# Performance work log

Measured on AMD Instinct MI355X. Metric: run time of the kernel, lower is better.

Reference implementation:

```python
import jax, jax.numpy as jnp
import numpy as np

V, D, H, DK, DV = 60000, 300, 15, 20, 20
B, NH, NC, L = 128, 50, 5, 30
HD = H * DV  # 300, equals d_model
A = 200      # additive attention hidden dim


def _encode(x, Wq, Wk, Wv, Wp, bp, qv):
    # NRMS news/user encoder: MHSA over positions + additive attention pooling.
    # x: [B, L, D] -> [B, HD]
    b, l, _ = x.shape
    q = (x @ Wq).reshape(b, l, H, DK)
    k = (x @ Wk).reshape(b, l, H, DK)
    v = (x @ Wv).reshape(b, l, H, DV)
    scores = jnp.einsum('blhk,bmhk->bhlm', q, k) / jnp.sqrt(jnp.asarray(DK, x.dtype))
    attn = jax.nn.softmax(scores, axis=-1)
    ctx = jnp.einsum('bhlm,bmhv->blhv', attn, v).reshape(b, l, HD)
    a = jax.nn.softmax(jnp.tanh(ctx @ Wp + bp) @ qv, axis=-1)  # [b, l]
    return jnp.einsum('bl,blc->bc', a, ctx)

# vectorize over the per-position encoder axis (replaces the Python loop +
# incremental torch.cat): inputs [B, P, L, D], weights have leading dim P.
_encode_pos = jax.vmap(_encode, in_axes=(1, 0, 0, 0, 0, 0, 0), out_axes=1)


def setup_inputs() -> dict:
    key = jax.random.key(0)
    ks = jax.random.split(key, 24)

    def mk(k, shape, s=0.02):
        return s * jax.random.normal(k, shape, jnp.float32)

    inp = {
        'news_input': jax.random.randint(ks[0], (B, NH, L), 0, V),
        'candidates': jax.random.randint(ks[1], (B, NC, L), 0, V),
        'emb': mk(ks[2], (V, D), 0.1),
    }
    for name, n, base in [('his', NH, 3), ('cand', NC, 10), ('usr', 0, 17)]:
        sh = (n,) if n else ()
        kk = jax.random.split(ks[base], 6)
        inp[name + '_Wq'] = mk(kk[0], sh + (D, H * DK))
        inp[name + '_Wk'] = mk(kk[1], sh + (D, H * DK))
        inp[name + '_Wv'] = mk(kk[2], sh + (D, H * DV))
        inp[name + '_Wp'] = mk(kk[3], sh + (HD, A))
        inp[name + '_bp'] = mk(kk[4], sh + (A,))
        inp[name + '_qv'] = mk(kk[5], sh + (A,))
    return inp


def reference(news_input, candidates, emb,
              his_Wq, his_Wk, his_Wv, his_Wp, his_bp, his_qv,
              cand_Wq, cand_Wk, cand_Wv, cand_Wp, cand_bp, cand_qv,
              usr_Wq, usr_Wk, usr_Wv, usr_Wp, usr_bp, usr_qv):
    news_emb = emb[news_input]   # [B, 50, L, D]
    cand_emb = emb[candidates]   # [B, 5, L, D]
    news_enc = _encode_pos(news_emb, his_Wq, his_Wk, his_Wv, his_Wp, his_bp, his_qv)    # [B, 50, 300]
    cand_enc = _encode_pos(cand_emb, cand_Wq, cand_Wk, cand_Wv, cand_Wp, cand_bp, cand_qv)  # [B, 5, 300]
    user_rep = _encode(news_enc, usr_Wq, usr_Wk, usr_Wv, usr_Wp, usr_bp, usr_qv)        # [B, 300]
    scores = jnp.einsum('bd,bcd->bc', user_rep, cand_enc)  # bmm of [B,1,300] x [B,300,5]
    return jax.nn.softmax(scores, axis=-1)
```

## Files before the change

kernel.cpp:

```cpp
#include <hip/hip_runtime.h>
#include <math.h>

typedef __attribute__((ext_vector_type(8))) short short8;
typedef __attribute__((ext_vector_type(4))) short short4v;
typedef __attribute__((ext_vector_type(4))) float f32x4;

union U32S8 { unsigned u[4]; short8 s8; ushort e[8]; short4v h[2]; };

#define BATCH 128
#define NHIS  50
#define NCAND 5
#define KP    320
#define NQKV  1024
#define NWP   208
#define NQK   640
#define CTS   320
#define VOCAB 60000
#define SCALE 0.22360679774997896f

__device__ __forceinline__ ushort f2bf(float f) {
    union { float f; unsigned u; } v; v.f = f;
    return (ushort)((v.u + 0x7fffu + ((v.u >> 16) & 1u)) >> 16);
}
__device__ __forceinline__ unsigned pack2bf(float lo, float hi) {
    return (unsigned)f2bf(lo) | ((unsigned)f2bf(hi) << 16);
}
__device__ __forceinline__ float bf2f(ushort u) {
    union { float f; unsigned u; } v; v.u = ((unsigned)u) << 16;
    return v.f;
}

__device__ __forceinline__ void gl_lds16(const ushort* gsrc, ushort* ldst) {
    __builtin_amdgcn_global_load_lds(
        (const __attribute__((address_space(1))) unsigned int*)gsrc,
        (__attribute__((address_space(3))) unsigned int*)ldst,
        16, 0, 0);
}

__global__ void prep_emb(const float* __restrict__ emb, ushort* __restrict__ dst) {
    size_t gid = (size_t)blockIdx.x * 256 + threadIdx.x;
    size_t total8 = (size_t)VOCAB * (KP / 8);
    if (gid >= total8) return;
    size_t e0 = gid * 8;
    int row = (int)(e0 / KP);
    int c   = (int)(e0 - (size_t)row * KP);
    unsigned w[4] = {0, 0, 0, 0};
    if (c + 8 <= 300) {
        const float4* s = (const float4*)(emb + (size_t)row * 300 + c);
        float4 v0 = s[0], v1 = s[1];
        w[0] = pack2bf(v0.x, v0.y); w[1] = pack2bf(v0.z, v0.w);
        w[2] = pack2bf(v1.x, v1.y); w[3] = pack2bf(v1.z, v1.w);
    } else if (c < 300) {
        const float* s = emb + (size_t)row * 300;
        ushort tmp[8];
        #pragma unroll
        for (int i = 0; i < 8; ++i) tmp[i] = (c + i < 300) ? f2bf(s[c + i]) : (ushort)0;
        w[0] = tmp[0] | ((unsigned)tmp[1] << 16);
        w[1] = tmp[2] | ((unsigned)tmp[3] << 16);
        w[2] = tmp[4] | ((unsigned)tmp[5] << 16);
        w[3] = tmp[6] | ((unsigned)tmp[7] << 16);
    }
    *(unsigned*)(dst + e0)     = w[0];
    *(unsigned*)(dst + e0 + 2) = w[1];
    *(unsigned*)(dst + e0 + 4) = w[2];
    *(unsigned*)(dst + e0 + 6) = w[3];
}

__global__ void prep_qkv(const float* __restrict__ Wq, const float* __restrict__ Wk,
                         const float* __restrict__ Wv, ushort* __restrict__ dst, int P) {
    size_t i = (size_t)blockIdx.x * 256 + threadIdx.x;
    size_t total = (size_t)P * NQKV * KP;
    if (i >= total) return;
    int k = (int)(i % KP);
    int n = (int)((i / KP) % NQKV);
    int p = (int)(i / ((size_t)KP * NQKV));
    float v = 0.f;
    if (k < 300 && n < 900) {
        const float* W = (n < 300) ? Wq : (n < 600 ? Wk : Wv);
        int nn = n % 300;
        v = W[((size_t)p * 300 + k) * 300 + nn];
    }
    dst[i] = f2bf(v);
}

__global__ void prep_wp(const float* __restrict__ Wp, ushort* __restrict__ dst, int P) {
    size_t i = (size_t)blockIdx.x * 256 + threadIdx.x;
    size_t total = (size_t)P * NWP * KP;
    if (i >= total) return;
    int k = (int)(i % KP);
    int a = (int)((i / KP) % NWP);
    int p = (int)(i / ((size_t)KP * NWP));
    float v = 0.f;
    if (k < 300 && a < 200) v = Wp[((size_t)p * 300 + k) * 200 + a];
    dst[i] = f2bf(v);
}

template<int LQ, bool GATHER>
__global__ __launch_bounds__(256, 4)
void qkv_gemm(const ushort* __restrict__ src_bf,
              const int* __restrict__ tokens,
              const ushort* __restrict__ wt,
              ushort* __restrict__ qk, ushort* __restrict__ vt,
              int p0, int P_all, int NPMT)
{
    constexpr int MT = (LQ == 30) ? 30 : 50;
    constexpr int VS = (LQ == 30) ? 32 : 64;
    constexpr int TS = 136;

    __shared__ __align__(16) char SM[34816];
    __shared__ int TOK[128];

    const int group = blockIdx.x >> 6;
    const int w64   = blockIdx.x & 63;
    const int mt_g  = group * 8 + (w64 & 7);
    const int ntile = w64 >> 3;
    if (mt_g >= NPMT) return;
    const int mtile = mt_g % MT;
    const int p_l   = mt_g / MT;
    const int p_g   = p0 + p_l;
    const int t     = threadIdx.x;
    const int wave  = t >> 6, lane = t & 63;
    const int r = lane & 15, g = lane >> 4;
    const int qm = wave >> 1, qn = wave & 1;

    if (GATHER && t < 128) {
        int row = mtile * 128 + t;
        int b = row / LQ, l = row - b * LQ;
        TOK[t] = tokens[((size_t)b * P_all + p_g) * LQ + l];
    }
    __syncthreads();

    const int kcs   = (lane & 3) ^ ((lane >> 2) & 3);
    const int rowA0 = wave * 16 + (lane >> 2);
    const int rowA1 = 64 + rowA0;
    const ushort* wtp = wt + (size_t)p_g * NQKV * KP;

    const ushort *pA0, *pA1;
    if (GATHER) {
        pA0 = src_bf + (size_t)TOK[rowA0] * KP + kcs * 8;
        pA1 = src_bf + (size_t)TOK[rowA1] * KP + kcs * 8;
    } else {
        pA0 = src_bf + (size_t)(mtile * 128 + rowA0) * KP + kcs * 8;
        pA1 = src_bf + (size_t)(mtile * 128 + rowA1) * KP + kcs * 8;
    }
    const ushort* pB0 = wtp + (size_t)(ntile * 128 + rowA0) * KP + kcs * 8;
    const ushort* pB1 = wtp + (size_t)(ntile * 128 + rowA1) * KP + kcs * 8;

    auto stage = [&](int ks, int bufb) {
        int ko = ks * 32;
        char* base = SM + bufb * 8192;
        gl_lds16(pA0 + ko, (ushort*)(base + wave * 1024));
        gl_lds16(pA1 + ko, (ushort*)(base + 4096 + wave * 1024));
        char* baseB = SM + 16384 + bufb * 8192;
        gl_lds16(pB0 + ko, (ushort*)(baseB + wave * 1024));
        gl_lds16(pB1 + ko, (ushort*)(baseB + 4096 + wave * 1024));
    };

    f32x4 acc[4][4];
    #pragma unroll
    for (int i = 0; i < 4; ++i)
        #pragma unroll
        for (int j = 0; j < 4; ++j)
            acc[i][j] = (f32x4){0.f, 0.f, 0.f, 0.f};

    stage(0, 0);
    __syncthreads();
    int buf = 0;
    const int kx = g ^ (r & 3);
    for (int ks = 0; ks < 10; ++ks) {
        if (ks < 9) stage(ks + 1, buf ^ 1);
        const ushort* Ab = (const ushort*)(SM + buf * 8192);
        const ushort* Bb = (const ushort*)(SM + 16384 + buf * 8192);
        short8 af[4], bfr[4];
        #pragma unroll
        for (int fi = 0; fi < 4; ++fi)
            af[fi] = *(const short8*)&Ab[(qm * 64 + fi * 16 + r) * 32 + kx * 8];
        #pragma unroll
        for (int fj = 0; fj < 4; ++fj)
            bfr[fj] = *(const short8*)&Bb[(qn * 64 + fj * 16 + r) * 32 + kx * 8];
        #pragma unroll
        for (int fi = 0; fi < 4; ++fi)
            #pragma unroll
            for (int fj = 0; fj < 4; ++fj)
                acc[fi][fj] = __builtin_amdgcn_mfma_f32_16x16x32_bf16(af[fi], bfr[fj], acc[fi][fj], 0, 0, 0);
        __syncthreads();
        buf ^= 1;
    }

    ushort* T = (ushort*)SM;
    #pragma unroll
    for (int fi = 0; fi < 4; ++fi) {
        #pragma unroll
        for (int fj = 0; fj < 4; ++fj) {
            int col  = qn * 64 + fj * 16 + r;
            int rowb = qm * 64 + fi * 16 + 4 * g;
            #pragma unroll
            for (int j = 0; j < 4; ++j)
                T[(rowb + j) * TS + col] = f2bf(acc[fi][fj][j]);
        }
    }
    __syncthreads();

    const int R0 = mtile * 128;
    const int N0 = ntile * 128;
    ushort* qkp = qk + (size_t)p_l * (128 * MT) * NQK;
    ushort* vtp = vt + (size_t)p_l * BATCH * 15 * 20 * VS;

    {
        int nqk = 600 - N0;
        if (nqk > 128) nqk = 128;
        if (nqk > 0) {
            int nch = nqk >> 3;
            for (int t2 = t; t2 < 128 * nch; t2 += 256) {
                int row = t2 / nch, cc = t2 - row * nch;
                short8 v = *(const short8*)&T[row * TS + cc * 8];
                *(short8*)&qkp[(size_t)(R0 + row) * NQK + N0 + cc * 8] = v;
            }
        }
    }
    {
        int c0 = 600 - N0; if (c0 < 0) c0 = 0;
        int c1 = 900 - N0; if (c1 > 128) c1 = 128;
        if (c1 > c0) {
            int nvt = c1 - c0;
            int b0 = R0 / LQ, b1 = (R0 + 127) / LQ;
            int nb = b1 - b0 + 1;
            for (int t2 = t; t2 < nvt * nb; t2 += 256) {
                int ci = t2 % nvt, bi = t2 / nvt;
                int c = c0 + ci;
                int vj = N0 + c - 600;
                int h = vj / 20, jj = vj - h * 20;
                int b = b0 + bi;
                int gr0 = b * LQ;      if (gr0 < R0) gr0 = R0;
                int gr1 = b * LQ + LQ; if (gr1 > R0 + 128) gr1 = R0 + 128;
                if (gr1 <= gr0) continue;
                int l0 = gr0 - b * LQ, l1 = gr1 - b * LQ;
                ushort* dst = vtp + (((size_t)b * 15 + h) * 20 + jj) * VS;
                int l = l0;
                while (l < l1) {
                    if ((l & 7) == 0 && l + 8 <= l1) {
                        U32S8 v;
                        #pragma unroll
                        for (int i = 0; i < 8; ++i)
                            v.e[i] = T[(b * LQ + l + i - R0) * TS + c];
                        *(short8*)&dst[l] = v.s8;
                        l += 8;
                    } else if ((l & 1) == 0 && l + 2 <= l1) {
                        unsigned v = (unsigned)T[(b * LQ + l - R0) * TS + c] |
                                     ((unsigned)T[(b * LQ + l + 1 - R0) * TS + c] << 16);
                        *(unsigned*)&dst[l] = v;
                        l += 2;
                    } else {
                        dst[l] = T[(b * LQ + l - R0) * TS + c];
                        l += 1;
                    }
                }
            }
        }
    }
}

__device__ __forceinline__ short8 load_qk_frag(const ushort* rowptr, int colbase, int g, bool rowvalid) {
    U32S8 v;
    v.s8 = (short8){0,0,0,0,0,0,0,0};
    if (rowvalid && g < 3) {
        const ushort* src = rowptr + colbase;
        if (g < 2) {
            v.h[0] = *(const short4v*)src;
            v.h[1] = *(const short4v*)(src + 4);
        } else {
            v.h[0] = *(const short4v*)src;
        }
    }
    return v.s8;
}

__global__ __launch_bounds__(256)
void attn_ctx(const ushort* __restrict__ qk,
              const ushort* __restrict__ vt,
              ushort* __restrict__ ctx,
              int)
{
    const int tid  = threadIdx.x;
    const int wave = tid >> 6;
    const int lane = tid & 63;
    const int r = lane & 15, g = lane >> 4;
    const int p_l = blockIdx.x / BATCH;
    const int b   = blockIdx.x % BATCH;

    const ushort* qb  = qk + ((size_t)p_l * BATCH + b) * 30 * NQK;
    const ushort* vb  = vt + ((size_t)p_l * BATCH + b) * 15 * 640;
    ushort* cb = ctx + ((size_t)p_l * BATCH + b) * 32 * CTS;

    for (int i = tid; i < 2 * CTS; i += 256) cb[30 * CTS + i] = 0;
    for (int i = tid; i < 32 * 20; i += 256) {
        int row = i / 20, c = 300 + i % 20;
        cb[row * CTS + c] = 0;
    }

    for (int hp = 0; hp < 4; ++hp) {
        int head = wave + 4 * hp;
        if (head < 15) {
            short8 q0 = load_qk_frag(qb + (size_t)(r) * NQK,      head * 20 + 8 * g, g, r < 30);
            short8 q1 = load_qk_frag(qb + (size_t)(16 + r) * NQK, head * 20 + 8 * g, g, 16 + r < 30);
            short8 k0 = load_qk_frag(qb + (size_t)(r) * NQK,      300 + head * 20 + 8 * g, g, r < 30);
            short8 k1 = load_qk_frag(qb + (size_t)(16 + r) * NQK, 300 + head * 20 + 8 * g, g, 16 + r < 30);
            short8 vf0 = *(const short8*)&vb[head * 640 + r * 32 + 8 * g];
            short8 vf1 = (16 + r < 20) ? *(const short8*)&vb[head * 640 + (16 + r) * 32 + 8 * g]
                                       : (short8){0,0,0,0,0,0,0,0};

            f32x4 s0m0 = {0,0,0,0}, s0m1 = {0,0,0,0}, s1m0 = {0,0,0,0}, s1m1 = {0,0,0,0};
            s0m0 = __builtin_amdgcn_mfma_f32_16x16x32_bf16(k0, q0, s0m0, 0, 0, 0);
            s0m1 = __builtin_amdgcn_mfma_f32_16x16x32_bf16(k1, q0, s0m1, 0, 0, 0);
            s1m0 = __builtin_amdgcn_mfma_f32_16x16x32_bf16(k0, q1, s1m0, 0, 0, 0);
            s1m1 = __builtin_amdgcn_mfma_f32_16x16x32_bf16(k1, q1, s1m1, 0, 0, 0);

            float mx0 = -1e30f, mx1 = -1e30f;
            #pragma unroll
            for (int j = 0; j < 4; ++j) {
                s0m0[j] *= SCALE; s1m0[j] *= SCALE;
                float v01 = (16 + 4 * g + j < 30) ? s0m1[j] * SCALE : -1e30f;
                float v11 = (16 + 4 * g + j < 30) ? s1m1[j] * SCALE : -1e30f;
                s0m1[j] = v01; s1m1[j] = v11;
                mx0 = fmaxf(mx0, fmaxf(s0m0[j], v01));
                mx1 = fmaxf(mx1, fmaxf(s1m0[j], v11));
            }
            mx0 = fmaxf(mx0, __shfl_xor(mx0, 16, 64));
            mx0 = fmaxf(mx0, __shfl_xor(mx0, 32, 64));
            mx1 = fmaxf(mx1, __shfl_xor(mx1, 16, 64));
            mx1 = fmaxf(mx1, __shfl_xor(mx1, 32, 64));
            float sm0 = 0.f, sm1 = 0.f;
            #pragma unroll
            for (int j = 0; j < 4; ++j) {
                s0m0[j] = __expf(s0m0[j] - mx0); s0m1[j] = __expf(s0m1[j] - mx0);
                s1m0[j] = __expf(s1m0[j] - mx1); s1m1[j] = __expf(s1m1[j] - mx1);
                sm0 += s0m0[j] + s0m1[j];
                sm1 += s1m0[j] + s1m1[j];
            }
            sm0 += __shfl_xor(sm0, 16, 64); sm0 += __shfl_xor(sm0, 32, 64);
            sm1 += __shfl_xor(sm1, 16, 64); sm1 += __shfl_xor(sm1, 32, 64);
            float inv0 = 1.0f / sm0, inv1 = 1.0f / sm1;

            unsigned pk000 = pack2bf(s0m0[0] * inv0, s0m0[1] * inv0);
            unsigned pk001 = pack2bf(s0m0[2] * inv0, s0m0[3] * inv0);
            unsigned pk010 = pack2bf(s0m1[0] * inv0, s0m1[1] * inv0);
            unsigned pk011 = pack2bf(s0m1[2] * inv0, s0m1[3] * inv0);
            unsigned pk100 = pack2bf(s1m0[0] * inv1, s1m0[1] * inv1);
            unsigned pk101 = pack2bf(s1m0[2] * inv1, s1m0[3] * inv1);
            unsigned pk110 = pack2bf(s1m1[0] * inv1, s1m1[1] * inv1);
            unsigned pk111 = pack2bf(s1m1[2] * inv1, s1m1[3] * inv1);

            const int sA = r + 16 * (2 * (g & 1));
            const int sB = sA + 16;
            const bool hi = (g >> 1) != 0;
            #pragma unroll
            for (int lt = 0; lt < 2; ++lt) {
                unsigned q00 = lt ? pk100 : pk000, q01 = lt ? pk101 : pk001;
                unsigned q10 = lt ? pk110 : pk010, q11 = lt ? pk111 : pk011;
                unsigned a0 = __shfl((int)q00, sA, 64), a1 = __shfl((int)q01, sA, 64);
                unsigned a2 = __shfl((int)q10, sA, 64), a3 = __shfl((int)q11, sA, 64);
                unsigned b0 = __shfl((int)q00, sB, 64), b1 = __shfl((int)q01, sB, 64);
                unsigned b2 = __shfl((int)q10, sB, 64), b3 = __shfl((int)q11, sB, 64);
                U32S8 pf;
                pf.u[0] = hi ? a2 : a0;
                pf.u[1] = hi ? a3 : a1;
                pf.u[2] = hi ? b2 : b0;
                pf.u[3] = hi ? b3 : b1;
                int lrow = lt * 16 + r;
                #pragma unroll
                for (int nt = 0; nt < 2; ++nt) {
                    short8 vf = nt ? vf1 : vf0;
                    f32x4 c = {0.f, 0.f, 0.f, 0.f};
                    c = __builtin_amdgcn_mfma_f32_16x16x32_bf16(vf, pf.s8, c, 0, 0, 0);
                    if (lrow < 30) {
                        #pragma unroll
                        for (int j = 0; j < 4; ++j) {
                            int vj = nt * 16 + 4 * g + j;
                            if (vj < 20)
                                cb[lrow * CTS + head * 20 + vj] = f2bf(c[j]);
                        }
                    }
                }
            }
        }
    }
}

__global__ __launch_bounds__(512, 1)
void attn50(const ushort* __restrict__ qk,
            const ushort* __restrict__ vt,
            ushort* __restrict__ ctx)
{
    __shared__ ushort P_l[8][64 * 68];

    const int tid  = threadIdx.x;
    const int wave = tid >> 6;
    const int lane = tid & 63;
    const int r = lane & 15, g = lane >> 4;
    const int b = blockIdx.x;

    const ushort* qb = qk + (size_t)b * 50 * NQK;
    ushort* pw = &P_l[wave][0];

    for (int hh = wave; hh < 15; hh += 8) {
        short8 qf[4], kf[4];
        #pragma unroll
        for (int t4 = 0; t4 < 4; ++t4) {
            qf[t4] = load_qk_frag(qb + (size_t)(t4 * 16 + r) * NQK, hh * 20 + 8 * g, g, true);
            kf[t4] = load_qk_frag(qb + (size_t)(t4 * 16 + r) * NQK, 300 + hh * 20 + 8 * g, g, true);
        }
        short8 vf[2][2];
        #pragma unroll
        for (int nt = 0; nt < 2; ++nt) {
            int vj = nt * 16 + r;
            #pragma unroll
            for (int ks = 0; ks < 2; ++ks) {
                if (vj < 20)
                    vf[nt][ks] = *(const short8*)&vt[(((size_t)b * 15 + hh) * 20 + vj) * 64 + ks * 32 + 8 * g];
                else
                    vf[nt][ks] = (short8){0,0,0,0,0,0,0,0};
            }
        }

        f32x4 s[4][4];
        #pragma unroll
        for (int qt = 0; qt < 4; ++qt)
            #pragma unroll
            for (int kt = 0; kt < 4; ++kt) {
                f32x4 z = {0.f, 0.f, 0.f, 0.f};
                s[qt][kt] = __builtin_amdgcn_mfma_f32_16x16x32_bf16(kf[kt], qf[qt], z, 0, 0, 0);
            }

        float mx[4], sm[4];
        #pragma unroll
        for (int qt = 0; qt < 4; ++qt) {
            float m = -1e30f;
            #pragma unroll
            for (int kt = 0; kt < 4; ++kt)
                #pragma unroll
                for (int j = 0; j < 4; ++j) {
                    int col = kt * 16 + 4 * g + j;
                    float v = (col < 50) ? s[qt][kt][j] * SCALE : -1e30f;
                    s[qt][kt][j] = v;
                    m = fmaxf(m, v);
                }
            m = fmaxf(m, __shfl_xor(m, 16, 64));
            m = fmaxf(m, __shfl_xor(m, 32, 64));
            mx[qt] = m;
            float sum = 0.f;
            #pragma unroll
            for (int kt = 0; kt < 4; ++kt)
                #pragma unroll
                for (int j = 0; j < 4; ++j) {
                    float e = __expf(s[qt][kt][j] - m);
                    s[qt][kt][j] = e;
                    sum += e;
                }
            sum += __shfl_xor(sum, 16, 64);
            sum += __shfl_xor(sum, 32, 64);
            sm[qt] = 1.0f / sum;
        }

        #pragma unroll
        for (int qt = 0; qt < 4; ++qt) {
            float inv = sm[qt];
            #pragma unroll
            for (int kt = 0; kt < 4; ++kt) {
                unsigned w0 = pack2bf(s[qt][kt][0] * inv, s[qt][kt][1] * inv);
                unsigned w1 = pack2bf(s[qt][kt][2] * inv, s[qt][kt][3] * inv);
                ushort* dst = pw + (qt * 16 + r) * 68 + kt * 16 + 4 * g;
                *(unsigned*)dst = w0;
                *(unsigned*)(dst + 2) = w1;
            }
        }
        asm volatile("s_waitcnt lgkmcnt(0)");
        __builtin_amdgcn_sched_barrier(0);

        #pragma unroll
        for (int lt = 0; lt < 4; ++lt) {
            short8 pf0 = *(const short8*)(pw + (lt * 16 + r) * 68 + 8 * g);
            short8 pf1 = *(const short8*)(pw + (lt * 16 + r) * 68 + 32 + 8 * g);
            int l = lt * 16 + r;
            #pragma unroll
            for (int nt = 0; nt < 2; ++nt) {
                f32x4 c = {0.f, 0.f, 0.f, 0.f};
                c = __builtin_amdgcn_mfma_f32_16x16x32_bf16(vf[nt][0], pf0, c, 0, 0, 0);
                c = __builtin_amdgcn_mfma_f32_16x16x32_bf16(vf[nt][1], pf1, c, 0, 0, 0);
                int vjb = nt * 16 + 4 * g;
                if (l < 50 && vjb < 17) {
                    unsigned w0 = pack2bf(c[0], c[1]);
                    unsigned w1 = pack2bf(c[2], c[3]);
                    ushort* d = ctx + ((size_t)b * 64 + l) * CTS + hh * 20 + vjb;
                    *(unsigned*)d = w0;
                    *(unsigned*)(d + 2) = w1;
                }
            }
        }
    }
}

template<bool BF16OUT>
__global__ __launch_bounds__(256, 2)
void pool_gemm(const ushort* __restrict__ ctx,
               const ushort* __restrict__ wt_wp,
               const float* __restrict__ bp, const float* __restrict__ qv,
               float* __restrict__ outf, ushort* __restrict__ outbf,
               int p0, int P_all)
{
    __shared__ ushort Bt[2][208 * 40];
    __shared__ float  logit[128];
    __shared__ float  aw[128];

    const int tid  = threadIdx.x;
    const int wave = tid >> 6;
    const int lane = tid & 63;
    const int r = lane & 15, g = lane >> 4;
    const int p_l   = blockIdx.x >> 5;
    const int mtile = blockIdx.x & 31;
    const int p_g   = p0 + p_l;

    const ushort* cbase = ctx + (size_t)p_l * BATCH * 32 * CTS + (size_t)mtile * 128 * CTS;
    const ushort* wpp = wt_wp + (size_t)p_g * NWP * KP;

    auto stageB = [&](int ks, int buf) {
        for (int i = tid; i < 832; i += 256) {
            int n = i >> 2, kk = (i & 3) * 8;
            *(short8*)&Bt[buf][n * 40 + kk] = *(const short8*)&wpp[(size_t)n * KP + ks * 32 + kk];
        }
    };

    float bpr[13], qvr[13];
    #pragma unroll
    for (int nf = 0; nf < 13; ++nf) {
        int col = nf * 16 + r;
        bpr[nf] = (col < 200) ? bp[p_g * 200 + col] : 0.f;
        qvr[nf] = (col < 200) ? qv[p_g * 200 + col] : 0.f;
    }

    f32x4 acc[2][13];
    #pragma unroll
    for (int mf = 0; mf < 2; ++mf)
        #pragma unroll
        for (int nf = 0; nf < 13; ++nf)
            acc[mf][nf] = (f32x4){0.f, 0.f, 0.f, 0.f};

    stageB(0, 0);
    __syncthreads();
    int buf = 0;
    for (int ks = 0; ks < 10; ++ks) {
        if (ks < 9) stageB(ks + 1, buf ^ 1);
        short8 af[2];
        #pragma unroll
        for (int mf = 0; mf < 2; ++mf)
            af[mf] = *(const short8*)&cbase[(size_t)(wave * 32 + mf * 16 + r) * CTS + ks * 32 + 8 * g];
        #pragma unroll
        for (int mf = 0; mf < 2; ++mf)
            #pragma unroll
            for (int nf = 0; nf < 13; ++nf) {
                short8 bf = *(const short8*)&Bt[buf][(nf * 16 + r) * 40 + 8 * g];
                acc[mf][nf] = __builtin_amdgcn_mfma_f32_16x16x32_bf16(af[mf], bf, acc[mf][nf], 0, 0, 0);
            }
        __syncthreads();
        buf ^= 1;
    }

    #pragma unroll
    for (int mf = 0; mf < 2; ++mf) {
        #pragma unroll
        for (int j = 0; j < 4; ++j) {
            float s = 0.f;
            #pragma unroll
            for (int nf = 0; nf < 13; ++nf)
                s += tanhf(acc[mf][nf][j] + bpr[nf]) * qvr[nf];
            s += __shfl_xor(s, 1, 64);
            s += __shfl_xor(s, 2, 64);
            s += __shfl_xor(s, 4, 64);
            s += __shfl_xor(s, 8, 64);
            if (r == 0) logit[wave * 32 + mf * 16 + 4 * g + j] = s;
        }
    }
    __syncthreads();

    {
        float x = (lane < 30) ? logit[wave * 32 + lane] : -1e30f;
        float mx = x;
        #pragma unroll
        for (int off = 1; off < 64; off <<= 1) mx = fmaxf(mx, __shfl_xor(mx, off, 64));
        float e = (lane < 30) ? __expf(x - mx) : 0.f;
        float sm = e;
        #pragma unroll
        for (int off = 1; off < 64; off <<= 1) sm += __shfl_xor(sm, off, 64);
        if (lane < 32) aw[wave * 32 + lane] = e / sm;
    }
    __syncthreads();

    for (int idx = tid; idx < 4 * 300; idx += 256) {
        int inst = idx / 300, c = idx - inst * 300;
        const ushort* crow = cbase + (size_t)inst * 32 * CTS + c;
        float o = 0.f;
        #pragma unroll
        for (int l = 0; l < 30; ++l)
            o = fmaf(aw[inst * 32 + l], bf2f(crow[(size_t)l * CTS]), o);
        int b = mtile * 4 + inst;
        if (BF16OUT) outbf[((size_t)b * P_all + p_g) * KP + c] = f2bf(o);
        else         outf[((size_t)b * P_all + p_g) * 300 + c] = o;
    }
}

__global__ __launch_bounds__(256, 2)
void pool50(const ushort* __restrict__ ctx,
            const ushort* __restrict__ wt_wp,
            const float* __restrict__ bp, const float* __restrict__ qv,
            float* __restrict__ user_rep)
{
    __shared__ ushort Bt[2][208 * 40];
    __shared__ float  logit[128];
    __shared__ float  aw[128];

    const int tid  = threadIdx.x;
    const int wave = tid >> 6;
    const int lane = tid & 63;
    const int r = lane & 15, g = lane >> 4;

    const ushort* cbase = ctx + (size_t)blockIdx.x * 2 * 64 * CTS;

    auto stageB = [&](int ks, int buf) {
        for (int i = tid; i < 832; i += 256) {
            int n = i >> 2, kk = (i & 3) * 8;
            *(short8*)&Bt[buf][n * 40 + kk] = *(const short8*)&wt_wp[(size_t)n * KP + ks * 32 + kk];
        }
    };

    float bpr[13], qvr[13];
    #pragma unroll
    for (int nf = 0; nf < 13; ++nf) {
        int col = nf * 16 + r;
        bpr[nf] = (col < 200) ? bp[col] : 0.f;
        qvr[nf] = (col < 200) ? qv[col] : 0.f;
    }

    f32x4 acc[2][13];
    #pragma unroll
    for (int mf = 0; mf < 2; ++mf)
        #pragma unroll
        for (int nf = 0; nf < 13; ++nf)
            acc[mf][nf] = (f32x4){0.f, 0.f, 0.f, 0.f};

    stageB(0, 0);
    __syncthreads();
    int buf = 0;
    for (int ks = 0; ks < 10; ++ks) {
        if (ks < 9) stageB(ks + 1, buf ^ 1);
        short8 af[2];
        #pragma unroll
        for (int mf = 0; mf < 2; ++mf)
            af[mf] = *(const short8*)&cbase[(size_t)(wave * 32 + mf * 16 + r) * CTS + ks * 32 + 8 * g];
        #pragma unroll
        for (int mf = 0; mf < 2; ++mf)
            #pragma unroll
            for (int nf = 0; nf < 13; ++nf) {
                short8 bf = *(const short8*)&Bt[buf][(nf * 16 + r) * 40 + 8 * g];
                acc[mf][nf] = __builtin_amdgcn_mfma_f32_16x16x32_bf16(af[mf], bf, acc[mf][nf], 0, 0, 0);
            }
        __syncthreads();
        buf ^= 1;
    }

    #pragma unroll
    for (int mf = 0; mf < 2; ++mf) {
        #pragma unroll
        for (int j = 0; j < 4; ++j) {
            float s = 0.f;
            #pragma unroll
            for (int nf = 0; nf < 13; ++nf)
                s += tanhf(acc[mf][nf][j] + bpr[nf]) * qvr[nf];
            s += __shfl_xor(s, 1, 64);
            s += __shfl_xor(s, 2, 64);
            s += __shfl_xor(s, 4, 64);
            s += __shfl_xor(s, 8, 64);
            if (r == 0) logit[wave * 32 + mf * 16 + 4 * g + j] = s;
        }
    }
    __syncthreads();

    if (wave < 2) {
        float x = (lane < 50) ? logit[wave * 64 + lane] : -1e30f;
        float mx = x;
        #pragma unroll
        for (int off = 1; off < 64; off <<= 1) mx = fmaxf(mx, __shfl_xor(mx, off, 64));
        float e = (lane < 50) ? __expf(x - mx) : 0.f;
        float sm = e;
        #pragma unroll
        for (int off = 1; off < 64; off <<= 1) sm += __shfl_xor(sm, off, 64);
        aw[wave * 64 + lane] = e / sm;
    }
    __syncthreads();

    for (int idx = tid; idx < 2 * 300; idx += 256) {
        int inst = idx / 300, c = idx - inst * 300;
        const ushort* crow = cbase + (size_t)inst * 64 * CTS + c;
        float o = 0.f;
        #pragma unroll
        for (int l = 0; l < 50; ++l)
            o = fmaf(aw[inst * 64 + l], bf2f(crow[(size_t)l * CTS]), o);
        int b = blockIdx.x * 2 + inst;
        user_rep[(size_t)b * 300 + c] = o;
    }
}

__global__ __launch_bounds__(320)
void score_kernel(const float* __restrict__ user_rep, const float* __restrict__ cand_enc,
                  float* __restrict__ out)
{
    __shared__ float sc[NCAND];
    int b = blockIdx.x;
    int w = threadIdx.x >> 6;
    int lane = threadIdx.x & 63;
    float partial = 0.f;
    for (int d = lane; d < 300; d += 64)
        partial = fmaf(user_rep[b * 300 + d], cand_enc[((size_t)b * NCAND + w) * 300 + d], partial);
    for (int off = 32; off > 0; off >>= 1)
        partial += __shfl_down(partial, off, 64);
    if (lane == 0) sc[w] = partial;
    __syncthreads();
    if (threadIdx.x == 0) {
        float mx = -1e30f;
        for (int c = 0; c < NCAND; ++c) mx = fmaxf(mx, sc[c]);
        float s = 0.f; float e[NCAND];
        for (int c = 0; c < NCAND; ++c) { e[c] = __expf(sc[c] - mx); s += e[c]; }
        float inv = 1.0f / s;
        for (int c = 0; c < NCAND; ++c) out[b * NCAND + c] = e[c] * inv;
    }
}

extern "C" void kernel_launch(void* const* d_in, const int* in_sizes, int n_in,
                              void* d_out, int out_size, void* d_ws, size_t ws_size,
                              hipStream_t stream) {
    const int*   news_input = (const int*)d_in[0];
    const int*   candidates = (const int*)d_in[1];
    const float* emb        = (const float*)d_in[2];
    const float* his_Wq  = (const float*)d_in[3];
    const float* his_Wk  = (const float*)d_in[4];
    const float* his_Wv  = (const float*)d_in[5];
    const float* his_Wp  = (const float*)d_in[6];
    const float* his_bp  = (const float*)d_in[7];
    const float* his_qv  = (const float*)d_in[8];
    const float* cand_Wq = (const float*)d_in[9];
    const float* cand_Wk = (const float*)d_in[10];
    const float* cand_Wv = (const float*)d_in[11];
    const float* cand_Wp = (const float*)d_in[12];
    const float* cand_bp = (const float*)d_in[13];
    const float* cand_qv = (const float*)d_in[14];
    const float* usr_Wq  = (const float*)d_in[15];
    const float* usr_Wk  = (const float*)d_in[16];
    const float* usr_Wv  = (const float*)d_in[17];
    const float* usr_Wp  = (const float*)d_in[18];
    const float* usr_bp  = (const float*)d_in[19];
    const float* usr_qv  = (const float*)d_in[20];
    float* out = (float*)d_out;

    char* ws = (char*)d_ws;
    ushort* emb_bf      = (ushort*)ws;            ws += (size_t)VOCAB * KP * 2;
    ushort* news_enc_bf = (ushort*)ws;            ws += (size_t)BATCH * NHIS * KP * 2;
    float* cand_enc = (float*)ws;                 ws += (size_t)BATCH * NCAND * 300 * 4;
    float* user_rep = (float*)ws;                 ws += (size_t)BATCH * 300 * 4;
    ushort* his_qkvT  = (ushort*)ws;              ws += (size_t)NHIS * NQKV * KP * 2;
    ushort* his_wpT   = (ushort*)ws;              ws += (size_t)NHIS * NWP  * KP * 2;
    ushort* cand_qkvT = (ushort*)ws;              ws += (size_t)NCAND * NQKV * KP * 2;
    ushort* cand_wpT  = (ushort*)ws;              ws += (size_t)NCAND * NWP  * KP * 2;
    ushort* usr_qkvT  = (ushort*)ws;              ws += (size_t)NQKV * KP * 2;
    ushort* usr_wpT   = (ushort*)ws;              ws += (size_t)NWP  * KP * 2;

    size_t used = (size_t)(ws - (char*)d_ws);
    size_t avail = (ws_size > used) ? (ws_size - used) : 0;
    size_t qk_pp  = (size_t)3840 * NQK * 2;
    size_t vt_pp  = (size_t)BATCH * 15 * 640 * 2;
    size_t ctx_pp = (size_t)BATCH * 32 * CTS * 2;
    size_t per_p  = qk_pp + vt_pp + ctx_pp;
    int CP = (int)(avail / per_p);
    if (CP > 50) CP = 50;
    if (CP < 3) CP = 3;

    ushort* qk_ws  = (ushort*)ws;
    ushort* vt_ws  = qk_ws + (size_t)CP * 3840 * NQK;
    ushort* ctx_ws = vt_ws + (size_t)CP * BATCH * 15 * 640;

    ushort* qk_u  = qk_ws;
    ushort* vt_u  = qk_u + (size_t)6400 * NQK;
    ushort* ctx_u = vt_u + (size_t)BATCH * 15 * 20 * 64;

    auto blocks = [](size_t total) { return (int)((total + 255) / 256); };
    auto qkv_grid = [](int npmt) { return ((npmt + 7) / 8) * 64; };

    hipMemsetAsync(news_enc_bf, 0, (size_t)BATCH * NHIS * KP * 2, stream);
    prep_emb<<<blocks((size_t)VOCAB * (KP / 8)), 256, 0, stream>>>(emb, emb_bf);
    prep_qkv<<<blocks((size_t)NHIS  * NQKV * KP), 256, 0, stream>>>(his_Wq,  his_Wk,  his_Wv,  his_qkvT,  NHIS);
    prep_qkv<<<blocks((size_t)NCAND * NQKV * KP), 256, 0, stream>>>(cand_Wq, cand_Wk, cand_Wv, cand_qkvT, NCAND);
    prep_qkv<<<blocks((size_t)1     * NQKV * KP), 256, 0, stream>>>(usr_Wq,  usr_Wk,  usr_Wv,  usr_qkvT,  1);
    prep_wp <<<blocks((size_t)NHIS  * NWP  * KP), 256, 0, stream>>>(his_Wp,  his_wpT,  NHIS);
    prep_wp <<<blocks((size_t)NCAND * NWP  * KP), 256, 0, stream>>>(cand_Wp, cand_wpT, NCAND);
    prep_wp <<<blocks((size_t)1     * NWP  * KP), 256, 0, stream>>>(usr_Wp,  usr_wpT,  1);

    for (int p0 = 0; p0 < NHIS; p0 += CP) {
        int cp = (NHIS - p0 < CP) ? (NHIS - p0) : CP;
        int npmt = cp * 30;
        qkv_gemm<30, true><<<qkv_grid(npmt), 256, 0, stream>>>(emb_bf, news_input, his_qkvT,
                                                               qk_ws, vt_ws, p0, NHIS, npmt);
        attn_ctx<<<cp * BATCH, 256, 0, stream>>>(qk_ws, vt_ws, ctx_ws, 0);
        pool_gemm<true><<<cp * 32, 256, 0, stream>>>(ctx_ws, his_wpT, his_bp, his_qv, nullptr, news_enc_bf, p0, NHIS);
    }
    {
        int npmt = NCAND * 30;
        qkv_gemm<30, true><<<qkv_grid(npmt), 256, 0, stream>>>(emb_bf, candidates, cand_qkvT,
                                                               qk_ws, vt_ws, 0, NCAND, npmt);
        attn_ctx<<<NCAND * BATCH, 256, 0, stream>>>(qk_ws, vt_ws, ctx_ws, 0);
        pool_gemm<false><<<NCAND * 32, 256, 0, stream>>>(ctx_ws, cand_wpT, cand_bp, cand_qv, cand_enc, nullptr, 0, NCAND);
    }

    hipMemsetAsync(vt_u, 0, (size_t)BATCH * 15 * 20 * 64 * 2, stream);
    qkv_gemm<50, false><<<qkv_grid(50), 256, 0, stream>>>(news_enc_bf, nullptr, usr_qkvT,
                                                          qk_u, vt_u, 0, 1, 50);
    attn50<<<BATCH, 512, 0, stream>>>(qk_u, vt_u, ctx_u);
    pool50<<<64, 256, 0, stream>>>(ctx_u, usr_wpT, usr_bp, usr_qv, user_rep);

    score_kernel<<<BATCH, 320, 0, stream>>>(user_rep, cand_enc, out);
}
```

Measured before the change: 985.9 us.

## Restructure additive-attention pooling to one block per instance with LDS-cached context

Replaces the pool_gemm kernel, where each block handled 4 batch instances with a double-buffered Wp tile staged in LDS, with pool_inst, where each block handles one (position, batch) instance. The instance's 32x300 context is staged once in LDS and reused for both the projection GEMM and the weighted sum. Wp columns are loaded straight into registers per wave, with 13 column tiles split across 4 waves, and the logits are reduced through LDS atomics. This launches 4x more, smaller blocks with lower register pressure (launch bounds 4) to raise occupancy and drop the strided global re-reads of ctx. In exchange, each block re-reads Wp from global/L2, and the work is unevenly split across waves (13 tiles over 4 waves).

```diff
diff --git a/kernel.cpp b/kernel.cpp
--- a/kernel.cpp
+++ b/kernel.cpp
@@ -500,89 +500,71 @@
 }
 
 template<bool BF16OUT>
-__global__ __launch_bounds__(256, 2)
-void pool_gemm(const ushort* __restrict__ ctx,
+__global__ __launch_bounds__(256, 4)
+void pool_inst(const ushort* __restrict__ ctx,
                const ushort* __restrict__ wt_wp,
                const float* __restrict__ bp, const float* __restrict__ qv,
                float* __restrict__ outf, ushort* __restrict__ outbf,
                int p0, int P_all)
 {
-    __shared__ ushort Bt[2][208 * 40];
-    __shared__ float  logit[128];
-    __shared__ float  aw[128];
+    constexpr int CS = 328;
+    __shared__ ushort C[32 * CS];
+    __shared__ float  SL[32];
+    __shared__ float  AW[32];
 
     const int tid  = threadIdx.x;
     const int wave = tid >> 6;
     const int lane = tid & 63;
     const int r = lane & 15, g = lane >> 4;
-    const int p_l   = blockIdx.x >> 5;
-    const int mtile = blockIdx.x & 31;
-    const int p_g   = p0 + p_l;
-
-    const ushort* cbase = ctx + (size_t)p_l * BATCH * 32 * CTS + (size_t)mtile * 128 * CTS;
+    const int p_l = blockIdx.x / BATCH;
+    const int b   = blockIdx.x % BATCH;
+    const int p_g = p0 + p_l;
+
+    const ushort* cb = ctx + ((size_t)p_l * BATCH + b) * 32 * CTS;
     const ushort* wpp = wt_wp + (size_t)p_g * NWP * KP;
 
-    auto stageB = [&](int ks, int buf) {
-        for (int i = tid; i < 832; i += 256) {
-            int n = i >> 2, kk = (i & 3) * 8;
-            *(short8*)&Bt[buf][n * 40 + kk] = *(const short8*)&wpp[(size_t)n * KP + ks * 32 + kk];
-        }
-    };
-
-    float bpr[13], qvr[13];
-    #pragma unroll
-    for (int nf = 0; nf < 13; ++nf) {
-        int col = nf * 16 + r;
-        bpr[nf] = (col < 200) ? bp[p_g * 200 + col] : 0.f;
-        qvr[nf] = (col < 200) ? qv[p_g * 200 + col] : 0.f;
-    }
-
-    f32x4 acc[2][13];
-    #pragma unroll
-    for (int mf = 0; mf < 2; ++mf)
-        #pragma unroll
-        for (int nf = 0; nf < 13; ++nf)
-            acc[mf][nf] = (f32x4){0.f, 0.f, 0.f, 0.f};
-
-    stageB(0, 0);
-    __syncthreads();
-    int buf = 0;
-    for (int ks = 0; ks < 10; ++ks) {
-        if (ks < 9) stageB(ks + 1, buf ^ 1);
-        short8 af[2];
-        #pragma unroll
-        for (int mf = 0; mf < 2; ++mf)
-            af[mf] = *(const short8*)&cbase[(size_t)(wave * 32 + mf * 16 + r) * CTS + ks * 32 + 8 * g];
-        #pragma unroll
-        for (int mf = 0; mf < 2; ++mf)
-            #pragma unroll
-            for (int nf = 0; nf < 13; ++nf) {
-                short8 bf = *(const short8*)&Bt[buf][(nf * 16 + r) * 40 + 8 * g];
-                acc[mf][nf] = __builtin_amdgcn_mfma_f32_16x16x32_bf16(af[mf], bf, acc[mf][nf], 0, 0, 0);
-            }
-        __syncthreads();
-        buf ^= 1;
-    }
-
-    #pragma unroll
-    for (int mf = 0; mf < 2; ++mf) {
+    for (int i = tid; i < 32 * 40; i += 256) {
+        int row = i / 40, cc = i - row * 40;
+        *(short8*)&C[row * CS + cc * 8] = *(const short8*)&cb[(size_t)row * CTS + cc * 8];
+    }
+    if (tid < 32) SL[tid] = 0.f;
+    __syncthreads();
+
+    for (int nt = wave; nt < 13; nt += 4) {
+        int col = nt * 16 + r;
+        const ushort* wrow = wpp + (size_t)col * KP + 8 * g;
+        short8 breg[10];
+        #pragma unroll
+        for (int ks = 0; ks < 10; ++ks) breg[ks] = *(const short8*)(wrow + 32 * ks);
+        float bpv = (col < 200) ? bp[p_g * 200 + col] : 0.f;
+        float qvv = (col < 200) ? qv[p_g * 200 + col] : 0.f;
+
+        f32x4 acc0 = {0.f, 0.f, 0.f, 0.f}, acc1 = {0.f, 0.f, 0.f, 0.f};
+        #pragma unroll
+        for (int ks = 0; ks < 10; ++ks) {
+            short8 a0 = *(const short8*)&C[(r) * CS + ks * 32 + 8 * g];
+            short8 a1 = *(const short8*)&C[(16 + r) * CS + ks * 32 + 8 * g];
+            acc0 = __builtin_amdgcn_mfma_f32_16x16x32_bf16(a0, breg[ks], acc0, 0, 0, 0);
+            acc1 = __builtin_amdgcn_mfma_f32_16x16x32_bf16(a1, breg[ks], acc1, 0, 0, 0);
+        }
         #pragma unroll
         for (int j = 0; j < 4; ++j) {
-            float s = 0.f;
-            #pragma unroll
-            for (int nf = 0; nf < 13; ++nf)
-                s += tanhf(acc[mf][nf][j] + bpr[nf]) * qvr[nf];
-            s += __shfl_xor(s, 1, 64);
-            s += __shfl_xor(s, 2, 64);
-            s += __shfl_xor(s, 4, 64);
-            s += __shfl_xor(s, 8, 64);
-            if (r == 0) logit[wave * 32 + mf * 16 + 4 * g + j] = s;
-        }
-    }
-    __syncthreads();
-
-    {
-        float x = (lane < 30) ? logit[wave * 32 + lane] : -1e30f;
+            float s0 = tanhf(acc0[j] + bpv) * qvv;
+            float s1 = tanhf(acc1[j] + bpv) * qvv;
+            s0 += __shfl_xor(s0, 1, 64); s1 += __shfl_xor(s1, 1, 64);
+            s0 += __shfl_xor(s0, 2, 64); s1 += __shfl_xor(s1, 2, 64);
+            s0 += __shfl_xor(s0, 4, 64); s1 += __shfl_xor(s1, 4, 64);
+            s0 += __shfl_xor(s0, 8, 64); s1 += __shfl_xor(s1, 8, 64);
+            if (r == 0) {
+                atomicAdd(&SL[4 * g + j], s0);
+                atomicAdd(&SL[16 + 4 * g + j], s1);
+            }
+        }
+    }
+    __syncthreads();
+
+    if (wave == 0) {
+        float x = (lane < 30) ? SL[lane] : -1e30f;
         float mx = x;
         #pragma unroll
         for (int off = 1; off < 64; off <<= 1) mx = fmaxf(mx, __shfl_xor(mx, off, 64));
@@ -590,18 +572,15 @@
         float sm = e;
         #pragma unroll
         for (int off = 1; off < 64; off <<= 1) sm += __shfl_xor(sm, off, 64);
-        if (lane < 32) aw[wave * 32 + lane] = e / sm;
-    }
-    __syncthreads();
-
-    for (int idx = tid; idx < 4 * 300; idx += 256) {
-        int inst = idx / 300, c = idx - inst * 300;
-        const ushort* crow = cbase + (size_t)inst * 32 * CTS + c;
+        if (lane < 32) AW[lane] = e / sm;
+    }
+    __syncthreads();
+
+    for (int c = tid; c < 300; c += 256) {
         float o = 0.f;
         #pragma unroll
         for (int l = 0; l < 30; ++l)
-            o = fmaf(aw[inst * 32 + l], bf2f(crow[(size_t)l * CTS]), o);
-        int b = mtile * 4 + inst;
+            o = fmaf(AW[l], bf2f(C[l * CS + c]), o);
         if (BF16OUT) outbf[((size_t)b * P_all + p_g) * KP + c] = f2bf(o);
         else         outf[((size_t)b * P_all + p_g) * 300 + c] = o;
     }
@@ -807,14 +786,16 @@
         qkv_gemm<30, true><<<qkv_grid(npmt), 256, 0, stream>>>(emb_bf, news_input, his_qkvT,
                                                                qk_ws, vt_ws, p0, NHIS, npmt);
         attn_ctx<<<cp * BATCH, 256, 0, stream>>>(qk_ws, vt_ws, ctx_ws, 0);
-        pool_gemm<true><<<cp * 32, 256, 0, stream>>>(ctx_ws, his_wpT, his_bp, his_qv, nullptr, news_enc_bf, p0, NHIS);
+        pool_inst<true><<<cp * BATCH, 256, 0, stream>>>(ctx_ws, his_wpT, his_bp, his_qv,
+                                                        nullptr, news_enc_bf, p0, NHIS);
     }
     {
         int npmt = NCAND * 30;
         qkv_gemm<30, true><<<qkv_grid(npmt), 256, 0, stream>>>(emb_bf, candidates, cand_qkvT,
                                                                qk_ws, vt_ws, 0, NCAND, npmt);
         attn_ctx<<<NCAND * BATCH, 256, 0, stream>>>(qk_ws, vt_ws, ctx_ws, 0);
-        pool_gemm<false><<<NCAND * 32, 256, 0, stream>>>(ctx_ws, cand_wpT, cand_bp, cand_qv, cand_enc, nullptr, 0, NCAND);
+        pool_inst<false><<<NCAND * BATCH, 256, 0, stream>>>(ctx_ws, cand_wpT, cand_bp, cand_qv,
+                                                            cand_enc, nullptr, 0, NCAND);
     }
 
     hipMemsetAsync(vt_u, 0, (size_t)BATCH * 15 * 20 * 64 * 2, stream);
```

Result: faster. 921.9 us (-6.5%).
